# Kernel optimization log

Measured on AMD Instinct MI355X. Metric: run time of the kernel, lower is better.

## Reference

```python
import jax, jax.numpy as jnp
import numpy as np

N_NODES = 50000
N_EDGES = 800000
N_GRAPHS = 512
NUM_TYPES = 1000
EMB = 128
HID = 128


def setup_inputs() -> dict:
    key = jax.random.key(0)
    ks = jax.random.split(key, 8)
    x_type = jax.random.randint(ks[0], (N_NODES,), 0, NUM_TYPES, dtype=jnp.int32)
    edge_index = jax.random.randint(ks[1], (2, N_EDGES), 0, N_NODES, dtype=jnp.int32)
    batch = jnp.sort(jax.random.randint(ks[2], (N_NODES,), 0, N_GRAPHS, dtype=jnp.int32))
    emb = jax.random.normal(ks[3], (NUM_TYPES, EMB), jnp.float32)
    s1 = 1.0 / np.sqrt(EMB)
    s2 = 1.0 / np.sqrt(HID)
    W1 = jax.random.normal(ks[4], (EMB, HID), jnp.float32) * s1
    b1 = jnp.zeros((HID,), jnp.float32)
    W2 = jax.random.normal(ks[5], (HID, HID), jnp.float32) * s2
    b2 = jnp.zeros((HID,), jnp.float32)
    return {"x_type": x_type, "edge_index": edge_index, "batch": batch,
            "emb": emb, "W1": W1, "b1": b1, "W2": W2, "b2": b2}


def _gcn_norm(edge_index, n_nodes):
    # PyG GCNConv default: add self-loops, symmetric normalization.
    loops = jnp.arange(n_nodes, dtype=edge_index.dtype)
    src = jnp.concatenate([edge_index[0], loops])  # [E+N]
    dst = jnp.concatenate([edge_index[1], loops])
    deg = jax.ops.segment_sum(jnp.ones_like(dst, jnp.float32), dst, num_segments=n_nodes)
    dis = jax.lax.rsqrt(deg)  # deg >= 1 thanks to self-loops
    norm = dis[src] * dis[dst]  # [E+N]
    return src, dst, norm


def _gcn_conv(x, src, dst, norm, W, b, n_nodes):
    h = x @ W                                  # [N, out]
    msg = h[src] * norm[:, None]               # edge-gathered, normalized messages
    out = jax.ops.segment_sum(msg, dst, num_segments=n_nodes)  # scatter-add
    return out + b


def reference(x_type, edge_index, batch, emb, W1, b1, W2, b2):
    src, dst, norm = _gcn_norm(edge_index, N_NODES)
    x = emb[x_type]                            # [N, EMB]
    x = jax.nn.relu(_gcn_conv(x, src, dst, norm, W1, b1, N_NODES))
    x = _gcn_conv(x, src, dst, norm, W2, b2, N_NODES)
    # index_add_ pooling over graphs (dropout is identity in eval / p=0)
    out = jax.ops.segment_sum(x, batch, num_segments=N_GRAPHS)  # [G, HID]
    return out
```

## Files before the change

### kernel.cpp

```cpp
#include <hip/hip_runtime.h>

#define N_NODES 50000
#define N_EDGES 800000
#define N_GRAPHS 512
#define FDIM 128
#define NTYPES_PAD 1000

#define NBLK 128
#define CHUNK ((N_EDGES + NBLK - 1) / NBLK)
#define NQUAD (N_NODES / 4)
#define NPAIR (N_NODES / 2)
#define NPW 8
#define NW ((N_NODES + NPW - 1) / NPW)

constexpr int SCAN_TILE = 256;
constexpr int NB = (N_NODES + SCAN_TILE - 1) / SCAN_TILE;

typedef __bf16 bf16x8 __attribute__((ext_vector_type(8)));
typedef float f32x4 __attribute__((ext_vector_type(4)));
union BF8 { bf16x8 v; unsigned short u[8]; };

__device__ __forceinline__ unsigned short f2bf(float f) {
  unsigned int u = __float_as_uint(f);
  unsigned int r = (u + 0x7FFFu + ((u >> 16) & 1u)) >> 16;
  return (unsigned short)r;
}
__device__ __forceinline__ float bflo(unsigned int v) {
  return __uint_as_float(v << 16);
}
__device__ __forceinline__ float bfhi(unsigned int v) {
  return __uint_as_float(v & 0xFFFF0000u);
}

__global__ void k_init(float* __restrict__ Zb) {
  int i = blockIdx.x * blockDim.x + threadIdx.x;
  if (i < N_GRAPHS * FDIM) Zb[i] = 0.0f;
}

__global__ __launch_bounds__(512) void k_hist(const int* __restrict__ dst,
                                              unsigned int* __restrict__ Hist,
                                              unsigned char* __restrict__ rank8) {
  __shared__ unsigned int h[NQUAD];
  int b = blockIdx.x, t = threadIdx.x;
  for (int i = t; i < NQUAD; i += 512) h[i] = 0;
  __syncthreads();
  int e0 = b * CHUNK, e1 = min(e0 + CHUNK, N_EDGES);
  for (int e = e0 + t; e < e1; e += 512) {
    int d = dst[e];
    unsigned int sh = (d & 3) * 8;
    unsigned int old = atomicAdd(&h[d >> 2], 1u << sh);
    rank8[e] = (unsigned char)((old >> sh) & 0xFFu);
  }
  __syncthreads();
  unsigned int* H = Hist + (size_t)b * NQUAD;
  for (int i = t; i < NQUAD; i += 512) H[i] = h[i];
}

__global__ void k_colscan(const unsigned int* __restrict__ Hist,
                          unsigned int* __restrict__ Cur, int* __restrict__ cnt,
                          float* __restrict__ dis) {
  int q = blockIdx.x * blockDim.x + threadIdx.x;
  if (q >= NQUAD) return;
  unsigned int r0 = 0, r1 = 0, r2 = 0, r3 = 0;
  for (int b = 0; b < NBLK; ++b) {
    unsigned int v = Hist[(size_t)b * NQUAD + q];
    Cur[(size_t)b * NPAIR + 2 * q] = r0 | (r1 << 16);
    Cur[(size_t)b * NPAIR + 2 * q + 1] = r2 | (r3 << 16);
    r0 += v & 255u;
    r1 += (v >> 8) & 255u;
    r2 += (v >> 16) & 255u;
    r3 += v >> 24;
  }
  int d = 4 * q;
  cnt[d] = r0; cnt[d + 1] = r1; cnt[d + 2] = r2; cnt[d + 3] = r3;
  dis[d] = rsqrtf((float)r0 + 1.f);
  dis[d + 1] = rsqrtf((float)r1 + 1.f);
  dis[d + 2] = rsqrtf((float)r2 + 1.f);
  dis[d + 3] = rsqrtf((float)r3 + 1.f);
}

__global__ void k_scan1(const int* __restrict__ cnt, int* __restrict__ row_ptr,
                        int* __restrict__ blk) {
  __shared__ int s[SCAN_TILE];
  int t = threadIdx.x;
  int i = blockIdx.x * SCAN_TILE + t;
  int v = (i < N_NODES) ? cnt[i] : 0;
  s[t] = v;
  __syncthreads();
  for (int d = 1; d < SCAN_TILE; d <<= 1) {
    int u = (t >= d) ? s[t - d] : 0;
    __syncthreads();
    s[t] += u;
    __syncthreads();
  }
  if (i < N_NODES) row_ptr[i] = s[t] - v;
  if (t == SCAN_TILE - 1) blk[blockIdx.x] = s[t];
}

__global__ void k_scan2(int* __restrict__ blk) {
  __shared__ int s[256];
  int t = threadIdx.x;
  int v = (t < NB) ? blk[t] : 0;
  s[t] = v;
  __syncthreads();
  for (int d = 1; d < 256; d <<= 1) {
    int u = (t >= d) ? s[t - d] : 0;
    __syncthreads();
    s[t] += u;
    __syncthreads();
  }
  if (t < NB) blk[t] = s[t] - v;
}

__global__ void k_scan3(int* __restrict__ row_ptr, const int* __restrict__ blk) {
  int i = blockIdx.x * blockDim.x + threadIdx.x;
  if (i < N_NODES) row_ptr[i] += blk[blockIdx.x];
  if (i == 0) row_ptr[N_NODES] = N_EDGES;
}

__global__ __launch_bounds__(512) void k_fill2(
    const int* __restrict__ src, const int* __restrict__ dst,
    const int* __restrict__ x_type, const int* __restrict__ row_ptr,
    const unsigned int* __restrict__ Cur, const unsigned char* __restrict__ rank8,
    const float* __restrict__ dis, int2* __restrict__ csr_t,
    int2* __restrict__ csr_s) {
  int e = blockIdx.x * blockDim.x + threadIdx.x;
  if (e >= N_EDGES) return;
  int b = e / CHUNK;
  int s = src[e], d = dst[e];
  unsigned int cw = Cur[(size_t)b * NPAIR + (d >> 1)];
  int base = (int)((cw >> ((d & 1) * 16)) & 0xFFFFu);
  int pos = row_ptr[d] + base + (int)rank8[e];
  int nb = __float_as_int(dis[s] * dis[d]);
  csr_t[pos] = make_int2(x_type[s], nb);
  csr_s[pos] = make_int2(s, nb);
}

__global__ void k_gstart(const int* __restrict__ batch,
                         int* __restrict__ gstart) {
  int i = blockIdx.x * blockDim.x + threadIdx.x;
  if (i >= N_NODES) return;
  int b = batch[i];
  int prev = (i == 0) ? -1 : batch[i - 1];
  for (int g = prev + 1; g <= b; ++g) gstart[g] = i;
  if (i == N_NODES - 1)
    for (int g = b + 1; g <= N_GRAPHS; ++g) gstart[g] = N_NODES;
}

__global__ void k_prep_w(const float* __restrict__ W,
                         unsigned short* __restrict__ Wt) {
  int id = blockIdx.x * blockDim.x + threadIdx.x;
  int k = id >> 7, n = id & 127;
  Wt[n * 128 + (k ^ ((n & 15) << 3))] = f2bf(W[k * 128 + n]);
}

__global__ __launch_bounds__(256) void k_embw(
    const float* __restrict__ emb, const unsigned short* __restrict__ Wt,
    unsigned short* __restrict__ T1) {
  __shared__ unsigned short Ws[128 * 128];
  int t = threadIdx.x, w = t >> 6, l = t & 63;
  {
    const float4* g = (const float4*)Wt;
    float4* ls = (float4*)Ws;
    for (int i = t; i < 2048; i += 256) ls[i] = g[i];
  }
  int row0 = blockIdx.x * 64 + w * 16;
  int arow = row0 + (l & 15);
  bool ok = arow < NTYPES_PAD;
  bf16x8 a[4];
#pragma unroll
  for (int ks = 0; ks < 4; ++ks) {
    BF8 av;
    const float* ap = emb + (size_t)arow * FDIM + (l >> 4) * 8 + ks * 32;
#pragma unroll
    for (int i = 0; i < 8; ++i) av.u[i] = ok ? f2bf(ap[i]) : 0;
    a[ks] = av.v;
  }
  __syncthreads();
  f32x4 acc[8] = {};
#pragma unroll
  for (int ks = 0; ks < 4; ++ks) {
#pragma unroll
    for (int ct = 0; ct < 8; ++ct) {
      int n = ct * 16 + (l & 15);
      int kk = (ks * 32 + (l >> 4) * 8) ^ ((n & 15) << 3);
      bf16x8 b = *(const bf16x8*)&Ws[n * 128 + kk];
      acc[ct] =
          __builtin_amdgcn_mfma_f32_16x16x32_bf16(a[ks], b, acc[ct], 0, 0, 0);
    }
  }
#pragma unroll
  for (int ct = 0; ct < 8; ++ct) {
    int col = ct * 16 + (l & 15);
#pragma unroll
    for (int r = 0; r < 4; ++r) {
      int row = row0 + (l >> 4) * 4 + r;
      if (row < NTYPES_PAD) T1[row * FDIM + col] = f2bf(acc[ct][r]);
    }
  }
}

__global__ void k_agg1(const int* __restrict__ x_type,
                       const unsigned short* __restrict__ T1,
                       const float* __restrict__ b1,
                       const int* __restrict__ row_ptr,
                       const int2* __restrict__ csr_t,
                       const float* __restrict__ dis,
                       unsigned int* __restrict__ y1) {
  int gid = blockIdx.x * blockDim.x + threadIdx.x;
  int node = gid >> 6;
  int lane = gid & 63;
  if (node >= N_NODES) return;
  const unsigned int* T = (const unsigned int*)T1;
  float di = dis[node];
  float w0 = di * di;
  unsigned int v = T[(size_t)x_type[node] * 64 + lane];
  float ax = bflo(v) * w0, ay = bfhi(v) * w0;
  int j = row_ptr[node], end = row_ptr[node + 1];
  for (; j + 4 <= end; j += 4) {
    int2 e0 = csr_t[j], e1 = csr_t[j + 1], e2 = csr_t[j + 2], e3 = csr_t[j + 3];
    unsigned int u0 = T[(size_t)e0.x * 64 + lane];
    unsigned int u1 = T[(size_t)e1.x * 64 + lane];
    unsigned int u2 = T[(size_t)e2.x * 64 + lane];
    unsigned int u3 = T[(size_t)e3.x * 64 + lane];
    float n0 = __int_as_float(e0.y), n1 = __int_as_float(e1.y);
    float n2 = __int_as_float(e2.y), n3 = __int_as_float(e3.y);
    ax = fmaf(bflo(u0), n0, ax); ay = fmaf(bfhi(u0), n0, ay);
    ax = fmaf(bflo(u1), n1, ax); ay = fmaf(bfhi(u1), n1, ay);
    ax = fmaf(bflo(u2), n2, ax); ay = fmaf(bfhi(u2), n2, ay);
    ax = fmaf(bflo(u3), n3, ax); ay = fmaf(bfhi(u3), n3, ay);
  }
  for (; j < end; ++j) {
    int2 e = csr_t[j];
    unsigned int u = T[(size_t)e.x * 64 + lane];
    float nw = __int_as_float(e.y);
    ax = fmaf(bflo(u), nw, ax);
    ay = fmaf(bfhi(u), nw, ay);
  }
  float2 bb = ((const float2*)b1)[lane];
  ax = fmaxf(ax + bb.x, 0.f);
  ay = fmaxf(ay + bb.y, 0.f);
  y1[(size_t)node * 64 + lane] = (unsigned int)f2bf(ax) |
                                 ((unsigned int)f2bf(ay) << 16);
}

__global__ void k_aggpool(const unsigned int* __restrict__ y1,
                          const int* __restrict__ row_ptr,
                          const int2* __restrict__ csr_s,
                          const float* __restrict__ dis,
                          const int* __restrict__ batch,
                          float* __restrict__ Partials, int* __restrict__ Gid,
                          float* __restrict__ Zb) {
  int gid = blockIdx.x * blockDim.x + threadIdx.x;
  int wid = gid >> 6;
  int lane = gid & 63;
  int n0 = wid * NPW;
  if (n0 >= N_NODES) return;
  int nend = min(n0 + NPW, N_NODES);
  int g0 = batch[n0];
  int gcur = g0;
  float px = 0.f, py = 0.f;
  float ax = 0.f, ay = 0.f;
  for (int node = n0; node < nend; ++node) {
    int g = batch[node];
    if (g != gcur) {
      if (gcur == g0) {
        px = ax; py = ay;
      } else {
        atomicAdd(&Zb[(size_t)gcur * FDIM + 2 * lane], ax);
        atomicAdd(&Zb[(size_t)gcur * FDIM + 2 * lane + 1], ay);
      }
      ax = 0.f; ay = 0.f;
      gcur = g;
    }
    float di = dis[node];
    float w0 = di * di;
    unsigned int v = y1[(size_t)node * 64 + lane];
    float sx = bflo(v) * w0, sy = bfhi(v) * w0;
    int j = row_ptr[node], end = row_ptr[node + 1];
    for (; j + 4 <= end; j += 4) {
      int2 e0 = csr_s[j], e1 = csr_s[j + 1];
      int2 e2 = csr_s[j + 2], e3 = csr_s[j + 3];
      unsigned int u0 = y1[(size_t)e0.x * 64 + lane];
      unsigned int u1 = y1[(size_t)e1.x * 64 + lane];
      unsigned int u2 = y1[(size_t)e2.x * 64 + lane];
      unsigned int u3 = y1[(size_t)e3.x * 64 + lane];
      float n0_ = __int_as_float(e0.y), n1_ = __int_as_float(e1.y);
      float n2_ = __int_as_float(e2.y), n3_ = __int_as_float(e3.y);
      sx = fmaf(bflo(u0), n0_, sx); sy = fmaf(bfhi(u0), n0_, sy);
      sx = fmaf(bflo(u1), n1_, sx); sy = fmaf(bfhi(u1), n1_, sy);
      sx = fmaf(bflo(u2), n2_, sx); sy = fmaf(bfhi(u2), n2_, sy);
      sx = fmaf(bflo(u3), n3_, sx); sy = fmaf(bfhi(u3), n3_, sy);
    }
    for (; j < end; ++j) {
      int2 e = csr_s[j];
      unsigned int u = y1[(size_t)e.x * 64 + lane];
      float nw = __int_as_float(e.y);
      sx = fmaf(bflo(u), nw, sx);
      sy = fmaf(bfhi(u), nw, sy);
    }
    ax += sx;
    ay += sy;
  }
  if (gcur == g0) {
    px = ax; py = ay;
  } else {
    atomicAdd(&Zb[(size_t)gcur * FDIM + 2 * lane], ax);
    atomicAdd(&Zb[(size_t)gcur * FDIM + 2 * lane + 1], ay);
  }
  ((float2*)Partials)[(size_t)wid * 64 + lane] = make_float2(px, py);
  if (lane == 0) Gid[wid] = g0;
}

__global__ __launch_bounds__(128) void k_poolzw2(
    const float* __restrict__ Partials, const int* __restrict__ Gid,
    const float* __restrict__ Zb, const int* __restrict__ gstart,
    const float* __restrict__ W2, const float* __restrict__ b2,
    float* __restrict__ out) {
  __shared__ float Zs[FDIM];
  int g = blockIdx.x, t = threadIdx.x;
  int s = gstart[g], e = gstart[g + 1];
  float acc = Zb[(size_t)g * FDIM + t];
  if (e > s) {
    int w0 = s / NPW, w1 = (e - 1) / NPW;
    for (int w = w0; w <= w1; ++w)
      if (Gid[w] == g) acc += Partials[(size_t)w * FDIM + t];
  }
  Zs[t] = acc;
  __syncthreads();
  float o = 0.f;
#pragma unroll 8
  for (int k = 0; k < FDIM; ++k) o = fmaf(Zs[k], W2[k * FDIM + t], o);
  out[(size_t)g * FDIM + t] = o + (float)(e - s) * b2[t];
}

extern "C" void kernel_launch(void* const* d_in, const int* in_sizes, int n_in,
                              void* d_out, int out_size, void* d_ws,
                              size_t ws_size, hipStream_t stream) {
  const int* x_type = (const int*)d_in[0];
  const int* edge_index = (const int*)d_in[1];
  const int* batch = (const int*)d_in[2];
  const float* emb = (const float*)d_in[3];
  const float* W1 = (const float*)d_in[4];
  const float* b1 = (const float*)d_in[5];
  const float* W2 = (const float*)d_in[6];
  const float* b2 = (const float*)d_in[7];
  float* out = (float*)d_out;

  const int* src = edge_index;
  const int* dst = edge_index + N_EDGES;

  char* p = (char*)d_ws;
  size_t off = 0;
  auto alloc = [&](size_t bytes) {
    void* r = p + off;
    off = (off + bytes + 255) & ~(size_t)255;
    return r;
  };
  float* dis = (float*)alloc(N_NODES * 4);
  int* cnt = (int*)alloc(N_NODES * 4);
  int* row_ptr = (int*)alloc((N_NODES + 1) * 4);
  int* blk = (int*)alloc(1024);
  int* gstart = (int*)alloc((N_GRAPHS + 1) * 4);
  unsigned int* Hist = (unsigned int*)alloc((size_t)NBLK * NQUAD * 4);
  unsigned int* Cur = (unsigned int*)alloc((size_t)NBLK * NPAIR * 4);
  unsigned char* rank8 = (unsigned char*)alloc(N_EDGES);
  int2* csr_t = (int2*)alloc((size_t)N_EDGES * 8);
  int2* csr_s = (int2*)alloc((size_t)N_EDGES * 8);
  unsigned short* Wt1 = (unsigned short*)alloc(128 * 128 * 2);
  unsigned short* T1 = (unsigned short*)alloc((size_t)NTYPES_PAD * FDIM * 2);
  unsigned int* y1 = (unsigned int*)alloc((size_t)N_NODES * 64 * 4);
  float* Partials = (float*)alloc((size_t)NW * FDIM * 4);
  int* Gid = (int*)alloc(NW * 4);
  float* Zb = (float*)alloc((size_t)N_GRAPHS * FDIM * 4);
  (void)ws_size;

  k_init<<<256, 256, 0, stream>>>(Zb);
  k_hist<<<NBLK, 512, 0, stream>>>(dst, Hist, rank8);
  k_colscan<<<(NQUAD + 255) / 256, 256, 0, stream>>>(Hist, Cur, cnt, dis);
  k_scan1<<<NB, 256, 0, stream>>>(cnt, row_ptr, blk);
  k_scan2<<<1, 256, 0, stream>>>(blk);
  k_scan3<<<NB, 256, 0, stream>>>(row_ptr, blk);
  k_fill2<<<(N_EDGES + 511) / 512, 512, 0, stream>>>(
      src, dst, x_type, row_ptr, Cur, rank8, dis, csr_t, csr_s);
  k_gstart<<<(N_NODES + 255) / 256, 256, 0, stream>>>(batch, gstart);
  k_prep_w<<<64, 256, 0, stream>>>(W1, Wt1);
  k_embw<<<(NTYPES_PAD + 63) / 64, 256, 0, stream>>>(emb, Wt1, T1);
  k_agg1<<<(N_NODES * 64 + 255) / 256, 256, 0, stream>>>(
      x_type, T1, b1, row_ptr, csr_t, dis, y1);
  k_aggpool<<<(NW * 64 + 255) / 256, 256, 0, stream>>>(
      y1, row_ptr, csr_s, dis, batch, Partials, Gid, Zb);
  k_poolzw2<<<N_GRAPHS, 128, 0, stream>>>(Partials, Gid, Zb, gstart, W2, b2,
                                          out);
}
```

Baseline: 176.8 us.

## Factor GCN normalization into node scaling and compress CSR edge arrays

The symmetric norm dis[s]*dis[d] is split into per-node scalings. Layer-1 outputs are prescaled by dis, so layer-2 aggregation becomes a plain sum over 16-bit source indices. Layer 1 reads a packed 32-bit word holding the source type and degree, and recomputes rsqrt per edge. Together this cuts CSR storage from two 8-byte arrays to one 4-byte and one 2-byte array. Separately, the gstart computation is folded into the init kernel, the W1 transpose is folded into the embedding GEMM, Cur prefix counts are packed to 8 bits, and nodes per wave in pooling drop from 8 to 4. The packing assumes node IDs and types fit in 16 bits and per-node prefix counts stay below 256.

```diff
diff --git a/kernel.cpp b/kernel.cpp
--- a/kernel.cpp
+++ b/kernel.cpp
@@ -9,8 +9,7 @@
 #define NBLK 128
 #define CHUNK ((N_EDGES + NBLK - 1) / NBLK)
 #define NQUAD (N_NODES / 4)
-#define NPAIR (N_NODES / 2)
-#define NPW 8
+#define NPW 4
 #define NW ((N_NODES + NPW - 1) / NPW)
 
 constexpr int SCAN_TILE = 256;
@@ -32,9 +31,16 @@
   return __uint_as_float(v & 0xFFFF0000u);
 }
 
-__global__ void k_init(float* __restrict__ Zb) {
+__global__ void k_misc(float* __restrict__ Zb, const int* __restrict__ batch,
+                       int* __restrict__ gstart) {
   int i = blockIdx.x * blockDim.x + threadIdx.x;
   if (i < N_GRAPHS * FDIM) Zb[i] = 0.0f;
+  if (i >= N_NODES) return;
+  int b = batch[i];
+  int prev = (i == 0) ? -1 : batch[i - 1];
+  for (int g = prev + 1; g <= b; ++g) gstart[g] = i;
+  if (i == N_NODES - 1)
+    for (int g = b + 1; g <= N_GRAPHS; ++g) gstart[g] = N_NODES;
 }
 
 __global__ __launch_bounds__(512) void k_hist(const int* __restrict__ dst,
@@ -57,26 +63,31 @@
 }
 
 __global__ void k_colscan(const unsigned int* __restrict__ Hist,
+                          const int* __restrict__ x_type,
                           unsigned int* __restrict__ Cur, int* __restrict__ cnt,
-                          float* __restrict__ dis) {
+                          float* __restrict__ dis,
+                          unsigned int* __restrict__ nodeinfo) {
   int q = blockIdx.x * blockDim.x + threadIdx.x;
   if (q >= NQUAD) return;
   unsigned int r0 = 0, r1 = 0, r2 = 0, r3 = 0;
   for (int b = 0; b < NBLK; ++b) {
     unsigned int v = Hist[(size_t)b * NQUAD + q];
-    Cur[(size_t)b * NPAIR + 2 * q] = r0 | (r1 << 16);
-    Cur[(size_t)b * NPAIR + 2 * q + 1] = r2 | (r3 << 16);
+    Cur[(size_t)b * NQUAD + q] =
+        (r0 & 255u) | ((r1 & 255u) << 8) | ((r2 & 255u) << 16) | (r3 << 24);
     r0 += v & 255u;
     r1 += (v >> 8) & 255u;
     r2 += (v >> 16) & 255u;
     r3 += v >> 24;
   }
   int d = 4 * q;
-  cnt[d] = r0; cnt[d + 1] = r1; cnt[d + 2] = r2; cnt[d + 3] = r3;
-  dis[d] = rsqrtf((float)r0 + 1.f);
-  dis[d + 1] = rsqrtf((float)r1 + 1.f);
-  dis[d + 2] = rsqrtf((float)r2 + 1.f);
-  dis[d + 3] = rsqrtf((float)r3 + 1.f);
+  ((int4*)cnt)[q] = make_int4(r0, r1, r2, r3);
+  float4 dv = make_float4(rsqrtf((float)r0 + 1.f), rsqrtf((float)r1 + 1.f),
+                          rsqrtf((float)r2 + 1.f), rsqrtf((float)r3 + 1.f));
+  ((float4*)dis)[q] = dv;
+  int4 xt = ((const int4*)x_type)[q];
+  ((uint4*)nodeinfo)[q] =
+      make_uint4((unsigned int)xt.x | (r0 << 16), (unsigned int)xt.y | (r1 << 16),
+                 (unsigned int)xt.z | (r2 << 16), (unsigned int)xt.w | (r3 << 16));
 }
 
 __global__ void k_scan1(const int* __restrict__ cnt, int* __restrict__ row_ptr,
@@ -120,49 +131,29 @@
 
 __global__ __launch_bounds__(512) void k_fill2(
     const int* __restrict__ src, const int* __restrict__ dst,
-    const int* __restrict__ x_type, const int* __restrict__ row_ptr,
-    const unsigned int* __restrict__ Cur, const unsigned char* __restrict__ rank8,
-    const float* __restrict__ dis, int2* __restrict__ csr_t,
-    int2* __restrict__ csr_s) {
+    const int* __restrict__ row_ptr, const unsigned int* __restrict__ Cur,
+    const unsigned char* __restrict__ rank8,
+    const unsigned int* __restrict__ nodeinfo, unsigned int* __restrict__ csr1,
+    unsigned short* __restrict__ csr2) {
   int e = blockIdx.x * blockDim.x + threadIdx.x;
   if (e >= N_EDGES) return;
   int b = e / CHUNK;
   int s = src[e], d = dst[e];
-  unsigned int cw = Cur[(size_t)b * NPAIR + (d >> 1)];
-  int base = (int)((cw >> ((d & 1) * 16)) & 0xFFFFu);
+  unsigned int cw = Cur[(size_t)b * NQUAD + (d >> 2)];
+  int base = (int)((cw >> ((d & 3) * 8)) & 0xFFu);
   int pos = row_ptr[d] + base + (int)rank8[e];
-  int nb = __float_as_int(dis[s] * dis[d]);
-  csr_t[pos] = make_int2(x_type[s], nb);
-  csr_s[pos] = make_int2(s, nb);
-}
-
-__global__ void k_gstart(const int* __restrict__ batch,
-                         int* __restrict__ gstart) {
-  int i = blockIdx.x * blockDim.x + threadIdx.x;
-  if (i >= N_NODES) return;
-  int b = batch[i];
-  int prev = (i == 0) ? -1 : batch[i - 1];
-  for (int g = prev + 1; g <= b; ++g) gstart[g] = i;
-  if (i == N_NODES - 1)
-    for (int g = b + 1; g <= N_GRAPHS; ++g) gstart[g] = N_NODES;
-}
-
-__global__ void k_prep_w(const float* __restrict__ W,
-                         unsigned short* __restrict__ Wt) {
-  int id = blockIdx.x * blockDim.x + threadIdx.x;
-  int k = id >> 7, n = id & 127;
-  Wt[n * 128 + (k ^ ((n & 15) << 3))] = f2bf(W[k * 128 + n]);
+  csr1[pos] = nodeinfo[s];
+  csr2[pos] = (unsigned short)s;
 }
 
 __global__ __launch_bounds__(256) void k_embw(
-    const float* __restrict__ emb, const unsigned short* __restrict__ Wt,
+    const float* __restrict__ emb, const float* __restrict__ W1,
     unsigned short* __restrict__ T1) {
   __shared__ unsigned short Ws[128 * 128];
   int t = threadIdx.x, w = t >> 6, l = t & 63;
-  {
-    const float4* g = (const float4*)Wt;
-    float4* ls = (float4*)Ws;
-    for (int i = t; i < 2048; i += 256) ls[i] = g[i];
+  for (int i = t; i < 16384; i += 256) {
+    int k = i >> 7, n = i & 127;
+    Ws[n * 128 + (k ^ ((n & 15) << 3))] = f2bf(W1[i]);
   }
   int row0 = blockIdx.x * 64 + w * 16;
   int arow = row0 + (l & 15);
@@ -200,11 +191,11 @@
   }
 }
 
-__global__ void k_agg1(const int* __restrict__ x_type,
+__global__ void k_agg1(const unsigned int* __restrict__ nodeinfo,
                        const unsigned short* __restrict__ T1,
                        const float* __restrict__ b1,
                        const int* __restrict__ row_ptr,
-                       const int2* __restrict__ csr_t,
+                       const unsigned int* __restrict__ csr1,
                        const float* __restrict__ dis,
                        unsigned int* __restrict__ y1) {
   int gid = blockIdx.x * blockDim.x + threadIdx.x;
@@ -213,40 +204,43 @@
   if (node >= N_NODES) return;
   const unsigned int* T = (const unsigned int*)T1;
   float di = dis[node];
-  float w0 = di * di;
-  unsigned int v = T[(size_t)x_type[node] * 64 + lane];
-  float ax = bflo(v) * w0, ay = bfhi(v) * w0;
+  unsigned int ni = nodeinfo[node];
+  unsigned int v = T[(size_t)(ni & 0xFFFFu) * 64 + lane];
+  float ax = bflo(v) * di, ay = bfhi(v) * di;
   int j = row_ptr[node], end = row_ptr[node + 1];
   for (; j + 4 <= end; j += 4) {
-    int2 e0 = csr_t[j], e1 = csr_t[j + 1], e2 = csr_t[j + 2], e3 = csr_t[j + 3];
-    unsigned int u0 = T[(size_t)e0.x * 64 + lane];
-    unsigned int u1 = T[(size_t)e1.x * 64 + lane];
-    unsigned int u2 = T[(size_t)e2.x * 64 + lane];
-    unsigned int u3 = T[(size_t)e3.x * 64 + lane];
-    float n0 = __int_as_float(e0.y), n1 = __int_as_float(e1.y);
-    float n2 = __int_as_float(e2.y), n3 = __int_as_float(e3.y);
+    unsigned int e0 = csr1[j], e1 = csr1[j + 1];
+    unsigned int e2 = csr1[j + 2], e3 = csr1[j + 3];
+    unsigned int u0 = T[(size_t)(e0 & 0xFFFFu) * 64 + lane];
+    unsigned int u1 = T[(size_t)(e1 & 0xFFFFu) * 64 + lane];
+    unsigned int u2 = T[(size_t)(e2 & 0xFFFFu) * 64 + lane];
+    unsigned int u3 = T[(size_t)(e3 & 0xFFFFu) * 64 + lane];
+    float n0 = rsqrtf((float)(e0 >> 16) + 1.f);
+    float n1 = rsqrtf((float)(e1 >> 16) + 1.f);
+    float n2 = rsqrtf((float)(e2 >> 16) + 1.f);
+    float n3 = rsqrtf((float)(e3 >> 16) + 1.f);
     ax = fmaf(bflo(u0), n0, ax); ay = fmaf(bfhi(u0), n0, ay);
     ax = fmaf(bflo(u1), n1, ax); ay = fmaf(bfhi(u1), n1, ay);
     ax = fmaf(bflo(u2), n2, ax); ay = fmaf(bfhi(u2), n2, ay);
     ax = fmaf(bflo(u3), n3, ax); ay = fmaf(bfhi(u3), n3, ay);
   }
   for (; j < end; ++j) {
-    int2 e = csr_t[j];
-    unsigned int u = T[(size_t)e.x * 64 + lane];
-    float nw = __int_as_float(e.y);
+    unsigned int e = csr1[j];
+    unsigned int u = T[(size_t)(e & 0xFFFFu) * 64 + lane];
+    float nw = rsqrtf((float)(e >> 16) + 1.f);
     ax = fmaf(bflo(u), nw, ax);
     ay = fmaf(bfhi(u), nw, ay);
   }
   float2 bb = ((const float2*)b1)[lane];
-  ax = fmaxf(ax + bb.x, 0.f);
-  ay = fmaxf(ay + bb.y, 0.f);
+  ax = fmaxf(fmaf(di, ax, bb.x), 0.f) * di;
+  ay = fmaxf(fmaf(di, ay, bb.y), 0.f) * di;
   y1[(size_t)node * 64 + lane] = (unsigned int)f2bf(ax) |
                                  ((unsigned int)f2bf(ay) << 16);
 }
 
 __global__ void k_aggpool(const unsigned int* __restrict__ y1,
                           const int* __restrict__ row_ptr,
-                          const int2* __restrict__ csr_s,
+                          const unsigned short* __restrict__ csr2,
                           const float* __restrict__ dis,
                           const int* __restrict__ batch,
                           float* __restrict__ Partials, int* __restrict__ Gid,
@@ -274,33 +268,25 @@
       gcur = g;
     }
     float di = dis[node];
-    float w0 = di * di;
     unsigned int v = y1[(size_t)node * 64 + lane];
-    float sx = bflo(v) * w0, sy = bfhi(v) * w0;
+    float sx = bflo(v), sy = bfhi(v);
     int j = row_ptr[node], end = row_ptr[node + 1];
     for (; j + 4 <= end; j += 4) {
-      int2 e0 = csr_s[j], e1 = csr_s[j + 1];
-      int2 e2 = csr_s[j + 2], e3 = csr_s[j + 3];
-      unsigned int u0 = y1[(size_t)e0.x * 64 + lane];
-      unsigned int u1 = y1[(size_t)e1.x * 64 + lane];
-      unsigned int u2 = y1[(size_t)e2.x * 64 + lane];
-      unsigned int u3 = y1[(size_t)e3.x * 64 + lane];
-      float n0_ = __int_as_float(e0.y), n1_ = __int_as_float(e1.y);
-      float n2_ = __int_as_float(e2.y), n3_ = __int_as_float(e3.y);
-      sx = fmaf(bflo(u0), n0_, sx); sy = fmaf(bfhi(u0), n0_, sy);
-      sx = fmaf(bflo(u1), n1_, sx); sy = fmaf(bfhi(u1), n1_, sy);
-      sx = fmaf(bflo(u2), n2_, sx); sy = fmaf(bfhi(u2), n2_, sy);
-      sx = fmaf(bflo(u3), n3_, sx); sy = fmaf(bfhi(u3), n3_, sy);
+      int s0 = csr2[j], s1 = csr2[j + 1], s2 = csr2[j + 2], s3 = csr2[j + 3];
+      unsigned int u0 = y1[(size_t)s0 * 64 + lane];
+      unsigned int u1 = y1[(size_t)s1 * 64 + lane];
+      unsigned int u2 = y1[(size_t)s2 * 64 + lane];
+      unsigned int u3 = y1[(size_t)s3 * 64 + lane];
+      sx += bflo(u0) + bflo(u1) + bflo(u2) + bflo(u3);
+      sy += bfhi(u0) + bfhi(u1) + bfhi(u2) + bfhi(u3);
     }
     for (; j < end; ++j) {
-      int2 e = csr_s[j];
-      unsigned int u = y1[(size_t)e.x * 64 + lane];
-      float nw = __int_as_float(e.y);
-      sx = fmaf(bflo(u), nw, sx);
-      sy = fmaf(bfhi(u), nw, sy);
-    }
-    ax += sx;
-    ay += sy;
+      unsigned int u = y1[(size_t)csr2[j] * 64 + lane];
+      sx += bflo(u);
+      sy += bfhi(u);
+    }
+    ax = fmaf(di, sx, ax);
+    ay = fmaf(di, sy, ay);
   }
   if (gcur == g0) {
     px = ax; py = ay;
@@ -362,12 +348,12 @@
   int* row_ptr = (int*)alloc((N_NODES + 1) * 4);
   int* blk = (int*)alloc(1024);
   int* gstart = (int*)alloc((N_GRAPHS + 1) * 4);
+  unsigned int* nodeinfo = (unsigned int*)alloc(N_NODES * 4);
   unsigned int* Hist = (unsigned int*)alloc((size_t)NBLK * NQUAD * 4);
-  unsigned int* Cur = (unsigned int*)alloc((size_t)NBLK * NPAIR * 4);
+  unsigned int* Cur = (unsigned int*)alloc((size_t)NBLK * NQUAD * 4);
   unsigned char* rank8 = (unsigned char*)alloc(N_EDGES);
-  int2* csr_t = (int2*)alloc((size_t)N_EDGES * 8);
-  int2* csr_s = (int2*)alloc((size_t)N_EDGES * 8);
-  unsigned short* Wt1 = (unsigned short*)alloc(128 * 128 * 2);
+  unsigned int* csr1 = (unsigned int*)alloc((size_t)N_EDGES * 4);
+  unsigned short* csr2 = (unsigned short*)alloc((size_t)N_EDGES * 2);
   unsigned short* T1 = (unsigned short*)alloc((size_t)NTYPES_PAD * FDIM * 2);
   unsigned int* y1 = (unsigned int*)alloc((size_t)N_NODES * 64 * 4);
   float* Partials = (float*)alloc((size_t)NW * FDIM * 4);
@@ -375,21 +361,20 @@
   float* Zb = (float*)alloc((size_t)N_GRAPHS * FDIM * 4);
   (void)ws_size;
 
-  k_init<<<256, 256, 0, stream>>>(Zb);
+  k_misc<<<256, 256, 0, stream>>>(Zb, batch, gstart);
   k_hist<<<NBLK, 512, 0, stream>>>(dst, Hist, rank8);
-  k_colscan<<<(NQUAD + 255) / 256, 256, 0, stream>>>(Hist, Cur, cnt, dis);
+  k_colscan<<<(NQUAD + 255) / 256, 256, 0, stream>>>(Hist, x_type, Cur, cnt,
+                                                     dis, nodeinfo);
   k_scan1<<<NB, 256, 0, stream>>>(cnt, row_ptr, blk);
   k_scan2<<<1, 256, 0, stream>>>(blk);
   k_scan3<<<NB, 256, 0, stream>>>(row_ptr, blk);
   k_fill2<<<(N_EDGES + 511) / 512, 512, 0, stream>>>(
-      src, dst, x_type, row_ptr, Cur, rank8, dis, csr_t, csr_s);
-  k_gstart<<<(N_NODES + 255) / 256, 256, 0, stream>>>(batch, gstart);
-  k_prep_w<<<64, 256, 0, stream>>>(W1, Wt1);
-  k_embw<<<(NTYPES_PAD + 63) / 64, 256, 0, stream>>>(emb, Wt1, T1);
+      src, dst, row_ptr, Cur, rank8, nodeinfo, csr1, csr2);
+  k_embw<<<(NTYPES_PAD + 63) / 64, 256, 0, stream>>>(emb, W1, T1);
   k_agg1<<<(N_NODES * 64 + 255) / 256, 256, 0, stream>>>(
-      x_type, T1, b1, row_ptr, csr_t, dis, y1);
+      nodeinfo, T1, b1, row_ptr, csr1, dis, y1);
   k_aggpool<<<(NW * 64 + 255) / 256, 256, 0, stream>>>(
-      y1, row_ptr, csr_s, dis, batch, Partials, Gid, Zb);
+      y1, row_ptr, csr2, dis, batch, Partials, Gid, Zb);
   k_poolzw2<<<N_GRAPHS, 128, 0, stream>>>(Partials, Gid, Zb, gstart, W2, b2,
                                           out);
 }
```

After: 169.3 us. 1.04x faster.
